# Kernel tuning notes

Hardware: AMD Instinct MI355X
Metric: run time of the kernel (lower is better)

The kernel has to match this reference:

```python
import jax, jax.numpy as jnp
import numpy as np

B, S, DIM, H = 2, 2048, 1024, 16
DH = DIM // H
ROPE_BASE = 10000.0
LOGIT_SCALE_INIT = 2.302585
EPS = 1e-6


def _rotate_half(x):
    # interleaved pairs: out[..., ::2] = -x[..., 1::2]; out[..., 1::2] = x[..., ::2]
    xr = x.reshape(x.shape[:-1] + (x.shape[-1] // 2, 2))
    out = jnp.stack([-xr[..., 1], xr[..., 0]], axis=-1)
    return out.reshape(x.shape)


def _rope_cos_sin(seq_len, head_dim, dtype):
    t = jnp.arange(seq_len, dtype=dtype)
    freqs = 1.0 / ROPE_BASE ** (jnp.arange(0, head_dim, 2, dtype=dtype) / head_dim)
    ang = t[:, None] * freqs[None, :]                # [S, Dh/2]
    emb = jnp.repeat(ang, 2, axis=-1)                # [S, Dh]
    return jnp.cos(emb)[None, None], jnp.sin(emb)[None, None]  # [1,1,S,Dh]


def _l2norm_last(x):
    return x / jnp.sqrt(jnp.sum(x * x, axis=-1, keepdims=True) + EPS)


def setup_inputs() -> dict:
    key = jax.random.key(0)
    ks = jax.random.split(key, 10)
    x = jax.random.normal(ks[0], (B, S, DIM), dtype=jnp.float32)
    # causal mask: True = masked (above diagonal)
    mask = jnp.broadcast_to(jnp.triu(jnp.ones((S, S), dtype=bool), k=1), (B, S, S))
    w = lambda k: jax.random.normal(k, (DIM, DIM), dtype=jnp.float32) * 0.02
    b = lambda k: jax.random.normal(k, (DIM,), dtype=jnp.float32) * 0.01
    return {
        "x": x,
        "Wq": w(ks[1]), "bq": b(ks[2]),
        "Wk": w(ks[3]), "bk": b(ks[4]),
        "Wv": w(ks[5]), "bv": b(ks[6]),
        "Wo": w(ks[7]), "bo": b(ks[8]),
        "logit_scale": jnp.float32(LOGIT_SCALE_INIT),
        "mask": mask,
    }


def reference(x, Wq, bq, Wk, bk, Wv, bv, Wo, bo, logit_scale, mask):
    Bx, Sx, Dm = x.shape
    Dh = Dm // H
    scale = Dh ** -0.5
    # projections (torch Linear: x @ W.T + b), split heads -> [B,H,S,Dh]
    q = (x @ Wq.T + bq).reshape(Bx, Sx, H, Dh).transpose(0, 2, 1, 3)
    k = (x @ Wk.T + bk).reshape(Bx, Sx, H, Dh).transpose(0, 2, 1, 3)
    v = (x @ Wv.T + bv).reshape(Bx, Sx, H, Dh).transpose(0, 2, 1, 3)
    cos, sin = _rope_cos_sin(Sx, Dh, x.dtype)
    q = q * cos + _rotate_half(q) * sin
    k = k * cos + _rotate_half(k) * sin
    q = _l2norm_last(q)
    k = _l2norm_last(k)
    scores = jnp.einsum('bhsd,bhtd->bhst', q, k) * scale * jnp.exp(logit_scale)
    scores = jnp.where(mask[:, None, :, :], -jnp.inf, scores)
    a = jax.nn.softmax(scores, axis=-1)
    out = jnp.einsum('bhst,bhtd->bhsd', a, v).transpose(0, 2, 1, 3).reshape(Bx, Sx, Dm)
    return out @ Wo.T + bo
```

## Files before the change

kernel.cpp:

```cpp
#include <hip/hip_runtime.h>
#include <hip/hip_bf16.h>
#include <math.h>

typedef __hip_bfloat16 bf16;
typedef __attribute__((ext_vector_type(8))) short short8;
typedef __attribute__((ext_vector_type(4))) float floatx4;

static constexpr int Bn = 2, Sn = 2048, Hn = 16, DHn = 64, DIMn = 1024;
static constexpr int Mn = Bn * Sn;

#if __has_builtin(__builtin_amdgcn_exp2f)
#define EXP2(x) __builtin_amdgcn_exp2f(x)
#else
#define EXP2(x) exp2f(x)
#endif

__device__ __forceinline__ unsigned short bfbits(float f) {
  union { __hip_bfloat16 h; unsigned short u; } cv;
  cv.h = __float2bfloat16(f);
  return cv.u;
}

__device__ __forceinline__ float bf2f(unsigned short u) {
  union { float f; unsigned int u; } cv;
  cv.u = ((unsigned int)u) << 16;
  return cv.f;
}

__device__ __forceinline__ void gload_lds16(const void* g, void* l) {
  __builtin_amdgcn_global_load_lds(
      (const __attribute__((address_space(1))) uint32_t*)g,
      (__attribute__((address_space(3))) uint32_t*)l, 16, 0, 0);
}

template <int N>
__device__ __forceinline__ void wait_vm() {
  if constexpr (N == 0) asm volatile("s_waitcnt vmcnt(0)" ::: "memory");
  else if constexpr (N == 2) asm volatile("s_waitcnt vmcnt(2)" ::: "memory");
  else if constexpr (N == 3) asm volatile("s_waitcnt vmcnt(3)" ::: "memory");
  else asm volatile("s_waitcnt vmcnt(4)" ::: "memory");
  __builtin_amdgcn_sched_barrier(0);
}

__global__ void prep_kernel(const float* __restrict__ x,
                            const float* __restrict__ a0, const float* __restrict__ a1,
                            const float* __restrict__ a2, const float* __restrict__ a3,
                            unsigned short* __restrict__ xo,
                            unsigned short* __restrict__ o0, unsigned short* __restrict__ o1,
                            unsigned short* __restrict__ o2, unsigned short* __restrict__ o3,
                            float* __restrict__ tc, float* __restrict__ ts) {
  const int bid = blockIdx.x;
  if (bid < 8192) {
    const float* s;
    unsigned short* d;
    int i;
    if (bid < 4096) {
      s = x; d = xo; i = bid * 256 + threadIdx.x;
    } else {
      int wsel = (bid - 4096) >> 10;
      s = (wsel == 0) ? a0 : (wsel == 1) ? a1 : (wsel == 2) ? a2 : a3;
      d = (wsel == 0) ? o0 : (wsel == 1) ? o1 : (wsel == 2) ? o2 : o3;
      i = ((bid - 4096) & 1023) * 256 + threadIdx.x;
    }
    float4 v = ((const float4*)s)[i];
    ushort4 o;
    o.x = bfbits(v.x); o.y = bfbits(v.y); o.z = bfbits(v.z); o.w = bfbits(v.w);
    ((ushort4*)d)[i] = o;
  } else {
    int t = (bid - 8192) * 256 + threadIdx.x;
    int pos = t >> 5, i = t & 31;
    float f = powf(10000.0f, -(float)i * (1.0f / 32.0f));
    float a = (float)pos * f;
    tc[t] = cosf(a);
    ts[t] = sinf(a);
  }
}

__global__ __launch_bounds__(256, 4) void qkv_kernel(
    const bf16* __restrict__ A,
    const bf16* __restrict__ Wq, const bf16* __restrict__ Wk, const bf16* __restrict__ Wv,
    const float* __restrict__ bq, const float* __restrict__ bk, const float* __restrict__ bv,
    const float* __restrict__ tc, const float* __restrict__ ts,
    unsigned short* __restrict__ qo, unsigned short* __restrict__ ko,
    unsigned short* __restrict__ vt) {
  __shared__ bf16 smem[16384];
  bf16* sAp = smem;
  bf16* sBp = smem + 8192;
  const int sel = blockIdx.y >> 4;
  const bf16* Bw = (sel == 0) ? Wq : (sel == 1) ? Wk : Wv;
  const float* bias = (sel == 0) ? bq : (sel == 1) ? bk : bv;
  const int tid = threadIdx.x;
  const int lane = tid & 63, wave = tid >> 6;
  const int fr = lane & 15, fq = lane >> 4;
  const int m0 = blockIdx.x * 64, n0 = (blockIdx.y & 15) * 64;

  floatx4 acc[4] = {};

  auto stage = [&](int buf, int k0) {
#pragma unroll
    for (int call = 0; call < 2; ++call) {
      int row = call * 32 + (tid >> 3);
      int sb = ((tid & 7) * 16) ^ ((row & 7) << 4);
      gload_lds16(A + (size_t)(m0 + row) * 1024 + k0 + sb / 2,
                  sAp + buf * 4096 + call * 2048 + wave * 512);
    }
#pragma unroll
    for (int call = 0; call < 2; ++call) {
      int row = call * 32 + (tid >> 3);
      int sb = ((tid & 7) * 16) ^ ((row & 7) << 4);
      gload_lds16(Bw + (size_t)(n0 + row) * 1024 + k0 + sb / 2,
                  sBp + buf * 4096 + call * 2048 + wave * 512);
    }
  };

  stage(0, 0);
  stage(1, 64);
  int cur = 0;
  for (int k0 = 0; k0 < 1024; k0 += 64) {
    if (k0 + 64 < 1024) wait_vm<4>(); else wait_vm<0>();
    __builtin_amdgcn_s_barrier();
    __builtin_amdgcn_sched_barrier(0);
    const char* sAc = (const char*)(sAp + cur * 4096);
    const char* sBc = (const char*)(sBp + cur * 4096);
    short8 af[2], bfr[4][2];
    {
      int arow = wave * 16 + fr;
      int asw = (arow & 7) << 4;
#pragma unroll
      for (int kc = 0; kc < 2; ++kc)
        af[kc] = *(const short8*)(sAc + arow * 128 + ((kc * 64 + fq * 16) ^ asw));
    }
#pragma unroll
    for (int ni = 0; ni < 4; ++ni) {
      int brow = ni * 16 + fr;
      int bsw = (brow & 7) << 4;
#pragma unroll
      for (int kc = 0; kc < 2; ++kc)
        bfr[ni][kc] = *(const short8*)(sBc + brow * 128 + ((kc * 64 + fq * 16) ^ bsw));
    }
#pragma unroll
    for (int ni = 0; ni < 4; ++ni)
#pragma unroll
      for (int kc = 0; kc < 2; ++kc)
        acc[ni] = __builtin_amdgcn_mfma_f32_16x16x32_bf16(af[kc], bfr[ni][kc], acc[ni], 0, 0, 0);
    __builtin_amdgcn_sched_barrier(0);
    __builtin_amdgcn_s_barrier();
    if (k0 + 128 < 1024) stage(cur, k0 + 128);
    cur ^= 1;
  }

  if (sel < 2) {
    unsigned short* dst = (sel == 0) ? qo : ko;
    const int h = n0 >> 6;
    float bias_d[4];
#pragma unroll
    for (int ni = 0; ni < 4; ++ni) bias_d[ni] = bias[n0 + ni * 16 + fr];
#pragma unroll
    for (int j = 0; j < 4; ++j) {
      int m = m0 + wave * 16 + fq * 4 + j;
      int b = m >> 11, srow = m & 2047;
      float y[4], ss = 0.f;
#pragma unroll
      for (int ni = 0; ni < 4; ++ni) {
        float val = acc[ni][j] + bias_d[ni];
        float prt = __shfl_xor(val, 1);
        int d = ni * 16 + fr;
        int jj = d >> 1;
        float cc = tc[srow * 32 + jj], sn = ts[srow * 32 + jj];
        y[ni] = (d & 1) ? (val * cc + prt * sn) : (val * cc - prt * sn);
        ss += y[ni] * y[ni];
      }
      ss += __shfl_xor(ss, 1);
      ss += __shfl_xor(ss, 2);
      ss += __shfl_xor(ss, 4);
      ss += __shfl_xor(ss, 8);
      float inv = rsqrtf(ss + 1e-6f);
      size_t ob = ((size_t)(b * 16 + h) * 2048 + srow) * 64;
#pragma unroll
      for (int ni = 0; ni < 4; ++ni)
        dst[ob + ni * 16 + fr] = bfbits(y[ni] * inv);
    }
  } else {
    char* ct = (char*)smem;
#pragma unroll
    for (int ni = 0; ni < 4; ++ni) {
      int nl = ni * 16 + fr;
      float bi = bias[n0 + nl];
#pragma unroll
      for (int j = 0; j < 4; j += 2) {
        int ml = wave * 16 + fq * 4 + j;
        unsigned int u = (unsigned int)bfbits(acc[ni][j] + bi) |
                         ((unsigned int)bfbits(acc[ni][j + 1] + bi) << 16);
        *(unsigned int*)(ct + nl * 128 + ((ml * 2) ^ ((nl & 7) << 4))) = u;
      }
    }
    __syncthreads();
    int nl2 = tid >> 2, ch = tid & 3;
    int dd = nl2;
    int h = n0 >> 6;
    int b = m0 >> 11, s0 = m0 & 2047;
    unsigned short* orow = vt + (((size_t)b * 16 + h) * 64 + dd) * 2048 + s0;
    {
      int mb = ch * 16;
      short8 v8a = *(const short8*)(ct + nl2 * 128 + ((mb * 2) ^ ((nl2 & 7) << 4)));
      short8 v8b = *(const short8*)(ct + nl2 * 128 + (((mb + 8) * 2) ^ ((nl2 & 7) << 4)));
      *(short8*)(orow + mb) = v8a;
      *(short8*)(orow + mb + 8) = v8b;
    }
  }
}

__global__ __launch_bounds__(256, 4) void gemm_bt_kernel(
    const bf16* __restrict__ A, const bf16* __restrict__ Bw,
    const float* __restrict__ bias, float* __restrict__ Cf) {
  __shared__ bf16 smem[16384];
  bf16* sAp = smem;
  bf16* sBp = smem + 8192;
  const int tid = threadIdx.x;
  const int lane = tid & 63, wave = tid >> 6;
  const int fr = lane & 15, fq = lane >> 4;
  const int m0 = blockIdx.x * 64, n0 = blockIdx.y * 64;

  floatx4 acc[4] = {};

  auto stage = [&](int buf, int k0) {
#pragma unroll
    for (int call = 0; call < 2; ++call) {
      int row = call * 32 + (tid >> 3);
      int sb = ((tid & 7) * 16) ^ ((row & 7) << 4);
      gload_lds16(A + (size_t)(m0 + row) * 1024 + k0 + sb / 2,
                  sAp + buf * 4096 + call * 2048 + wave * 512);
    }
#pragma unroll
    for (int call = 0; call < 2; ++call) {
      int row = call * 32 + (tid >> 3);
      int sb = ((tid & 7) * 16) ^ ((row & 7) << 4);
      gload_lds16(Bw + (size_t)(n0 + row) * 1024 + k0 + sb / 2,
                  sBp + buf * 4096 + call * 2048 + wave * 512);
    }
  };

  stage(0, 0);
  stage(1, 64);
  int cur = 0;
  for (int k0 = 0; k0 < 1024; k0 += 64) {
    if (k0 + 64 < 1024) wait_vm<4>(); else wait_vm<0>();
    __builtin_amdgcn_s_barrier();
    __builtin_amdgcn_sched_barrier(0);
    const char* sAc = (const char*)(sAp + cur * 4096);
    const char* sBc = (const char*)(sBp + cur * 4096);
    short8 af[2], bfr[4][2];
    {
      int arow = wave * 16 + fr;
      int asw = (arow & 7) << 4;
#pragma unroll
      for (int kc = 0; kc < 2; ++kc)
        af[kc] = *(const short8*)(sAc + arow * 128 + ((kc * 64 + fq * 16) ^ asw));
    }
#pragma unroll
    for (int ni = 0; ni < 4; ++ni) {
      int brow = ni * 16 + fr;
      int bsw = (brow & 7) << 4;
#pragma unroll
      for (int kc = 0; kc < 2; ++kc)
        bfr[ni][kc] = *(const short8*)(sBc + brow * 128 + ((kc * 64 + fq * 16) ^ bsw));
    }
#pragma unroll
    for (int ni = 0; ni < 4; ++ni)
#pragma unroll
      for (int kc = 0; kc < 2; ++kc)
        acc[ni] = __builtin_amdgcn_mfma_f32_16x16x32_bf16(af[kc], bfr[ni][kc], acc[ni], 0, 0, 0);
    __builtin_amdgcn_sched_barrier(0);
    __builtin_amdgcn_s_barrier();
    if (k0 + 128 < 1024) stage(cur, k0 + 128);
    cur ^= 1;
  }

#pragma unroll
  for (int ni = 0; ni < 4; ++ni) {
    int n = n0 + ni * 16 + fr;
    float bi = bias[n];
#pragma unroll
    for (int j = 0; j < 4; ++j) {
      int m = m0 + wave * 16 + fq * 4 + j;
      Cf[(size_t)m * 1024 + n] = acc[ni][j] + bi;
    }
  }
}

__global__ __launch_bounds__(256, 4) void attn_kernel(
    const bf16* __restrict__ qb, const bf16* __restrict__ kb, const bf16* __restrict__ vt,
    const float* __restrict__ ls, unsigned short* __restrict__ out) {
  __shared__ bf16 sK[2][64 * 64];
  __shared__ bf16 sV[2][64 * 64];
  __shared__ char p_lds[4][2048];
  const int bid = blockIdx.x;
  const int rr4 = bid >> 8, g = bid & 255, jj = g & 31;
  const int xq = (rr4 & 1) ? (31 - jj) : jj;
  const int bh = (g >> 5) + 8 * rr4;
  const int q0A = xq * 32, q0B = (63 - xq) * 32;
  const int tid = threadIdx.x;
  const int lane = tid & 63, wave = tid >> 6;
  const int fr = lane & 15, fq = lane >> 4;
  const int myq0 = ((((wave >> 1) ^ bid) & 1)) ? q0B : q0A;
  const int base = myq0 + (wave & 1) * 16;
  float scl2 = __expf(ls[0]) * 0.125f * 1.44269504f;

  const size_t qrow = (size_t)bh * 2048 + base + fr;
  short8 qf0 = *(const short8*)(qb + qrow * 64 + fq * 8);
  short8 qf1 = *(const short8*)(qb + qrow * 64 + 32 + fq * 8);
  asm volatile("" : "+v"(qf0), "+v"(qf1), "+v"(scl2));
  __builtin_amdgcn_sched_barrier(0);

  const bf16* kgb = kb + (size_t)bh * 2048 * 64;
  const bf16* vgb = vt + (size_t)bh * 64 * 2048;

  auto stage = [&](int buf, int t0) {
#pragma unroll
    for (int call = 0; call < 2; ++call) {
      int row = call * 32 + (tid >> 3);
      int sb = ((tid & 7) * 16) ^ ((row & 7) << 4);
      gload_lds16(kgb + (size_t)(t0 + row) * 64 + sb / 2,
                  &sK[buf][call * 2048 + wave * 512]);
    }
#pragma unroll
    for (int call = 0; call < 2; ++call) {
      int row = call * 32 + (tid >> 3);
      int sb = ((tid & 7) * 16) ^ ((row & 7) << 4);
      gload_lds16(vgb + (size_t)row * 2048 + t0 + sb / 2,
                  &sV[buf][call * 2048 + wave * 512]);
    }
  };

  floatx4 oacc[4] = {};
  float mb2[4], lrun[4];
#pragma unroll
  for (int r = 0; r < 4; ++r) { mb2[r] = -INFINITY; lrun[r] = 0.f; }
  const int rowq = base + fq * 4;
  const int sw = (fr & 7) << 4;
  char* pw = p_lds[wave];
  short8 onesf;
#pragma unroll
  for (int i = 0; i < 8; ++i) onesf[i] = 0x3F80;

  const int tEnd = q0B + 32;
  stage(0, 0);
  stage(1, 64);
  int cur = 0;
  for (int t0 = 0; t0 < tEnd; t0 += 64) {
    if (t0 + 64 < tEnd) wait_vm<4>(); else wait_vm<0>();
    __builtin_amdgcn_s_barrier();
    __builtin_amdgcn_sched_barrier(0);
    if (t0 < myq0 + 32) {
      const char* sKc = (const char*)sK[cur];
      const char* sVc = (const char*)sV[cur];
      floatx4 sacc[4] = {};
      __builtin_amdgcn_s_setprio(1);
#pragma unroll
      for (int c = 0; c < 4; ++c) {
        int rb = (c * 16 + fr) * 128;
        short8 kf0 = *(const short8*)(sKc + rb + ((fq * 16) ^ sw));
        short8 kf1 = *(const short8*)(sKc + rb + ((64 + fq * 16) ^ sw));
        sacc[c] = __builtin_amdgcn_mfma_f32_16x16x32_bf16(qf0, kf0, sacc[c], 0, 0, 0);
        sacc[c] = __builtin_amdgcn_mfma_f32_16x16x32_bf16(qf1, kf1, sacc[c], 0, 0, 0);
      }
      __builtin_amdgcn_s_setprio(0);
      if (t0 + 63 > rowq) {
#pragma unroll
        for (int c = 0; c < 4; ++c)
#pragma unroll
          for (int r = 0; r < 4; ++r)
            if ((t0 + c * 16 + fr) > (rowq + r)) sacc[c][r] = -1e30f;
      }
      float pl[4];
#pragma unroll
      for (int r = 0; r < 4; ++r)
        pl[r] = fmaxf(fmaxf(sacc[0][r], sacc[1][r]), fmaxf(sacc[2][r], sacc[3][r]));
      float cmax = -INFINITY;
#pragma unroll
      for (int r = 0; r < 4; ++r) cmax = fmaxf(cmax, pl[r] * scl2 - mb2[r]);
      if (!__all(cmax <= 11.5f)) {
#pragma unroll
        for (int r = 0; r < 4; ++r) {
          float pm = pl[r];
#pragma unroll
          for (int msk = 1; msk < 16; msk <<= 1) pm = fmaxf(pm, __shfl_xor(pm, msk));
          float mnew = fmaxf(mb2[r], pm * scl2);
          float rs = EXP2(mb2[r] - mnew);
          mb2[r] = mnew;
          lrun[r] *= rs;
#pragma unroll
          for (int d = 0; d < 4; ++d) oacc[d][r] *= rs;
        }
      }
#pragma unroll
      for (int c = 0; c < 4; ++c)
#pragma unroll
        for (int r = 0; r < 4; ++r) {
          union { float f; unsigned int u; } pu;
          pu.f = EXP2(sacc[c][r] * scl2 - mb2[r]);
          int prow = fq * 4 + r;
          *(unsigned short*)(pw + prow * 128 + ((c * 32 + 2 * fr) ^ ((prow & 7) << 4))) =
              (unsigned short)(pu.u >> 16);
        }
      short8 pf0 = *(const short8*)(pw + fr * 128 + ((fq * 16) ^ sw));
      short8 pf1 = *(const short8*)(pw + fr * 128 + ((64 + fq * 16) ^ sw));
      __builtin_amdgcn_s_setprio(1);
      floatx4 tsum = {};
      tsum = __builtin_amdgcn_mfma_f32_16x16x32_bf16(pf0, onesf, tsum, 0, 0, 0);
      tsum = __builtin_amdgcn_mfma_f32_16x16x32_bf16(pf1, onesf, tsum, 0, 0, 0);
#pragma unroll
      for (int d = 0; d < 4; ++d) {
        int rb = (d * 16 + fr) * 128;
        short8 vf0 = *(const short8*)(sVc + rb + ((fq * 16) ^ sw));
        short8 vf1 = *(const short8*)(sVc + rb + ((64 + fq * 16) ^ sw));
        oacc[d] = __builtin_amdgcn_mfma_f32_16x16x32_bf16(pf0, vf0, oacc[d], 0, 0, 0);
        oacc[d] = __builtin_amdgcn_mfma_f32_16x16x32_bf16(pf1, vf1, oacc[d], 0, 0, 0);
      }
      __builtin_amdgcn_s_setprio(0);
#pragma unroll
      for (int r = 0; r < 4; ++r) lrun[r] += tsum[r];
    }
    __builtin_amdgcn_sched_barrier(0);
    __builtin_amdgcn_s_barrier();
    if (t0 + 128 < tEnd) stage(cur, t0 + 128);
    cur ^= 1;
  }
  const int b = bh >> 4, h = bh & 15;
#pragma unroll
  for (int r = 0; r < 4; ++r) {
    float il = 1.0f / lrun[r];
#pragma unroll
    for (int d = 0; d < 4; ++d) {
      size_t o = ((size_t)b * 2048 + rowq + r) * 1024 + h * 64 + d * 16 + fr;
      out[o] = bfbits(oacc[d][r] * il);
    }
  }
}

extern "C" void kernel_launch(void* const* d_in, const int* in_sizes, int n_in,
                              void* d_out, int out_size, void* d_ws, size_t ws_size,
                              hipStream_t stream) {
  (void)in_sizes; (void)n_in; (void)out_size; (void)ws_size;
  const float* x  = (const float*)d_in[0];
  const float* Wq = (const float*)d_in[1];
  const float* bq = (const float*)d_in[2];
  const float* Wk = (const float*)d_in[3];
  const float* bk = (const float*)d_in[4];
  const float* Wv = (const float*)d_in[5];
  const float* bv = (const float*)d_in[6];
  const float* Wo = (const float*)d_in[7];
  const float* bo = (const float*)d_in[8];
  const float* lsc = (const float*)d_in[9];

  uint8_t* w = (uint8_t*)d_ws;
  const size_t MB = 1ull << 20;
  bf16* xb   = (bf16*)(w + 0);
  bf16* wqb  = (bf16*)(w + 8 * MB);
  bf16* wkb  = (bf16*)(w + 10 * MB);
  bf16* wvb  = (bf16*)(w + 12 * MB);
  bf16* wob  = (bf16*)(w + 14 * MB);
  bf16* qbn  = (bf16*)(w + 16 * MB);
  bf16* kbn  = (bf16*)(w + 24 * MB);
  bf16* vtb  = (bf16*)(w + 32 * MB);
  bf16* atb  = (bf16*)(w + 40 * MB);
  float* tc  = (float*)(w + 48 * MB);
  float* ts  = (float*)(w + 48 * MB + 256 * 1024);

  prep_kernel<<<8448, 256, 0, stream>>>(
      x, Wq, Wk, Wv, Wo, (unsigned short*)xb,
      (unsigned short*)wqb, (unsigned short*)wkb, (unsigned short*)wvb,
      (unsigned short*)wob, tc, ts);

  qkv_kernel<<<dim3(64, 48), 256, 0, stream>>>(
      xb, wqb, wkb, wvb, bq, bk, bv, tc, ts,
      (unsigned short*)qbn, (unsigned short*)kbn, (unsigned short*)vtb);

  attn_kernel<<<1024, 256, 0, stream>>>(qbn, kbn, vtb, lsc,
                                        (unsigned short*)atb);

  gemm_bt_kernel<<<dim3(64, 16), 256, 0, stream>>>(atb, wob, bo, (float*)d_out);
}
```

Baseline: 117.2 us.

## Compute transposed scores in registers to feed PV MFMA without LDS round-trip

Swaps the MFMA operand order so each lane holds a column of S^T (one query row per lane group). The softmax probabilities can then be packed straight into bf16 register fragments for the P·V MFMA, removing the per-wave LDS scratch buffer, its writes and reads, and the ones-vector MFMA used for row sums. Row max and sum now use fewer cross-lane shuffles, with a shuffle to redistribute rescale factors. Launch bounds are raised to 5 blocks per CU because shared memory use drops. V is read with 8-byte LDS loads in a permuted k order, which may cost extra LDS instructions and register pressure.

```diff
diff --git a/kernel.cpp b/kernel.cpp
--- a/kernel.cpp
+++ b/kernel.cpp
@@ -25,6 +25,12 @@
   union { float f; unsigned int u; } cv;
   cv.u = ((unsigned int)u) << 16;
   return cv.f;
+}
+
+__device__ __forceinline__ unsigned int pack_bf16(float lo, float hi) {
+  union { float f; unsigned int u; } a, b;
+  a.f = lo; b.f = hi;
+  return (b.u & 0xFFFF0000u) | (a.u >> 16);
 }
 
 __device__ __forceinline__ void gload_lds16(const void* g, void* l) {
@@ -288,12 +294,11 @@
   }
 }
 
-__global__ __launch_bounds__(256, 4) void attn_kernel(
+__global__ __launch_bounds__(256, 5) void attn_kernel(
     const bf16* __restrict__ qb, const bf16* __restrict__ kb, const bf16* __restrict__ vt,
     const float* __restrict__ ls, unsigned short* __restrict__ out) {
   __shared__ bf16 sK[2][64 * 64];
   __shared__ bf16 sV[2][64 * 64];
-  __shared__ char p_lds[4][2048];
   const int bid = blockIdx.x;
   const int rr4 = bid >> 8, g = bid & 255, jj = g & 31;
   const int xq = (rr4 & 1) ? (31 - jj) : jj;
@@ -333,15 +338,10 @@
   };
 
   floatx4 oacc[4] = {};
-  float mb2[4], lrun[4];
-#pragma unroll
-  for (int r = 0; r < 4; ++r) { mb2[r] = -INFINITY; lrun[r] = 0.f; }
+  float m_l = -INFINITY, l_l = 0.f;
+  const int qrow_l = base + fr;
   const int rowq = base + fq * 4;
   const int sw = (fr & 7) << 4;
-  char* pw = p_lds[wave];
-  short8 onesf;
-#pragma unroll
-  for (int i = 0; i < 8; ++i) onesf[i] = 0x3F80;
 
   const int tEnd = q0B + 32;
   stage(0, 0);
@@ -361,65 +361,72 @@
         int rb = (c * 16 + fr) * 128;
         short8 kf0 = *(const short8*)(sKc + rb + ((fq * 16) ^ sw));
         short8 kf1 = *(const short8*)(sKc + rb + ((64 + fq * 16) ^ sw));
-        sacc[c] = __builtin_amdgcn_mfma_f32_16x16x32_bf16(qf0, kf0, sacc[c], 0, 0, 0);
-        sacc[c] = __builtin_amdgcn_mfma_f32_16x16x32_bf16(qf1, kf1, sacc[c], 0, 0, 0);
+        sacc[c] = __builtin_amdgcn_mfma_f32_16x16x32_bf16(kf0, qf0, sacc[c], 0, 0, 0);
+        sacc[c] = __builtin_amdgcn_mfma_f32_16x16x32_bf16(kf1, qf1, sacc[c], 0, 0, 0);
       }
       __builtin_amdgcn_s_setprio(0);
-      if (t0 + 63 > rowq) {
+      if (t0 + 63 > base) {
 #pragma unroll
         for (int c = 0; c < 4; ++c)
 #pragma unroll
           for (int r = 0; r < 4; ++r)
-            if ((t0 + c * 16 + fr) > (rowq + r)) sacc[c][r] = -1e30f;
-      }
-      float pl[4];
-#pragma unroll
-      for (int r = 0; r < 4; ++r)
-        pl[r] = fmaxf(fmaxf(sacc[0][r], sacc[1][r]), fmaxf(sacc[2][r], sacc[3][r]));
-      float cmax = -INFINITY;
-#pragma unroll
-      for (int r = 0; r < 4; ++r) cmax = fmaxf(cmax, pl[r] * scl2 - mb2[r]);
-      if (!__all(cmax <= 11.5f)) {
+            if ((t0 + c * 16 + fq * 4 + r) > qrow_l) sacc[c][r] = -1e30f;
+      }
+      float pm0 = fmaxf(fmaxf(sacc[0][0], sacc[0][1]), fmaxf(sacc[0][2], sacc[0][3]));
+      float pm1 = fmaxf(fmaxf(sacc[1][0], sacc[1][1]), fmaxf(sacc[1][2], sacc[1][3]));
+      float pm2 = fmaxf(fmaxf(sacc[2][0], sacc[2][1]), fmaxf(sacc[2][2], sacc[2][3]));
+      float pm3 = fmaxf(fmaxf(sacc[3][0], sacc[3][1]), fmaxf(sacc[3][2], sacc[3][3]));
+      float pm = fmaxf(fmaxf(pm0, pm1), fmaxf(pm2, pm3));
+      if (!__all(pm * scl2 - m_l <= 11.5f)) {
+        float pmr = fmaxf(pm, __shfl_xor(pm, 16));
+        pmr = fmaxf(pmr, __shfl_xor(pmr, 32));
+        float mnew = fmaxf(m_l, pmr * scl2);
+        float rs = EXP2(m_l - mnew);
+        m_l = mnew;
+        l_l *= rs;
+        float rsr[4];
+#pragma unroll
+        for (int r = 0; r < 4; ++r) rsr[r] = __shfl(rs, rowq - base + r);
+#pragma unroll
+        for (int d = 0; d < 4; ++d)
+#pragma unroll
+          for (int r = 0; r < 4; ++r) oacc[d][r] *= rsr[r];
+      }
+      float p[4][4];
+      float ssum = 0.f;
+#pragma unroll
+      for (int c = 0; c < 4; ++c)
 #pragma unroll
         for (int r = 0; r < 4; ++r) {
-          float pm = pl[r];
-#pragma unroll
-          for (int msk = 1; msk < 16; msk <<= 1) pm = fmaxf(pm, __shfl_xor(pm, msk));
-          float mnew = fmaxf(mb2[r], pm * scl2);
-          float rs = EXP2(mb2[r] - mnew);
-          mb2[r] = mnew;
-          lrun[r] *= rs;
-#pragma unroll
-          for (int d = 0; d < 4; ++d) oacc[d][r] *= rs;
+          p[c][r] = EXP2(sacc[c][r] * scl2 - m_l);
+          ssum += p[c][r];
         }
-      }
-#pragma unroll
-      for (int c = 0; c < 4; ++c)
-#pragma unroll
-        for (int r = 0; r < 4; ++r) {
-          union { float f; unsigned int u; } pu;
-          pu.f = EXP2(sacc[c][r] * scl2 - mb2[r]);
-          int prow = fq * 4 + r;
-          *(unsigned short*)(pw + prow * 128 + ((c * 32 + 2 * fr) ^ ((prow & 7) << 4))) =
-              (unsigned short)(pu.u >> 16);
+      ssum += __shfl_xor(ssum, 16);
+      ssum += __shfl_xor(ssum, 32);
+      l_l += ssum;
+      short8 pf[2];
+#pragma unroll
+      for (int kc = 0; kc < 2; ++kc) {
+        union { unsigned int w[4]; short8 v; } pk;
+        pk.w[0] = pack_bf16(p[kc][0], p[kc][1]);
+        pk.w[1] = pack_bf16(p[kc][2], p[kc][3]);
+        pk.w[2] = pack_bf16(p[kc + 2][0], p[kc + 2][1]);
+        pk.w[3] = pack_bf16(p[kc + 2][2], p[kc + 2][3]);
+        pf[kc] = pk.v;
+      }
+      __builtin_amdgcn_s_setprio(1);
+#pragma unroll
+      for (int d = 0; d < 4; ++d) {
+        int rbv = (d * 16 + fr) * 128;
+#pragma unroll
+        for (int kc = 0; kc < 2; ++kc) {
+          union { long long l[2]; short8 v; } vfu;
+          vfu.l[0] = *(const long long*)(sVc + rbv + ((kc * 32 + fq * 8) ^ sw));
+          vfu.l[1] = *(const long long*)(sVc + rbv + ((kc * 32 + fq * 8 + 64) ^ sw));
+          oacc[d] = __builtin_amdgcn_mfma_f32_16x16x32_bf16(pf[kc], vfu.v, oacc[d], 0, 0, 0);
         }
-      short8 pf0 = *(const short8*)(pw + fr * 128 + ((fq * 16) ^ sw));
-      short8 pf1 = *(const short8*)(pw + fr * 128 + ((64 + fq * 16) ^ sw));
-      __builtin_amdgcn_s_setprio(1);
-      floatx4 tsum = {};
-      tsum = __builtin_amdgcn_mfma_f32_16x16x32_bf16(pf0, onesf, tsum, 0, 0, 0);
-      tsum = __builtin_amdgcn_mfma_f32_16x16x32_bf16(pf1, onesf, tsum, 0, 0, 0);
-#pragma unroll
-      for (int d = 0; d < 4; ++d) {
-        int rb = (d * 16 + fr) * 128;
-        short8 vf0 = *(const short8*)(sVc + rb + ((fq * 16) ^ sw));
-        short8 vf1 = *(const short8*)(sVc + rb + ((64 + fq * 16) ^ sw));
-        oacc[d] = __builtin_amdgcn_mfma_f32_16x16x32_bf16(pf0, vf0, oacc[d], 0, 0, 0);
-        oacc[d] = __builtin_amdgcn_mfma_f32_16x16x32_bf16(pf1, vf1, oacc[d], 0, 0, 0);
       }
       __builtin_amdgcn_s_setprio(0);
-#pragma unroll
-      for (int r = 0; r < 4; ++r) lrun[r] += tsum[r];
     }
     __builtin_amdgcn_sched_barrier(0);
     __builtin_amdgcn_s_barrier();
@@ -427,13 +434,15 @@
     cur ^= 1;
   }
   const int b = bh >> 4, h = bh & 15;
+  float il[4];
+#pragma unroll
+  for (int r = 0; r < 4; ++r) il[r] = 1.0f / __shfl(l_l, rowq - base + r);
 #pragma unroll
   for (int r = 0; r < 4; ++r) {
-    float il = 1.0f / lrun[r];
 #pragma unroll
     for (int d = 0; d < 4; ++d) {
       size_t o = ((size_t)b * 2048 + rowq + r) * 1024 + h * 64 + d * 16 + fr;
-      out[o] = bfbits(oacc[d][r] * il);
+      out[o] = bfbits(oacc[d][r] * il[r]);
     }
   }
 }
```

After: 119.8 us. 1.02x slower.
